# Kernel optimization log

Hardware: AMD Instinct MI355X
Metric: run time of the kernel (lower is better)

The kernel has to match this reference:

```python
import jax, jax.numpy as jnp
import numpy as np

TOP_K = 50  # init default top_k=50
EPS = 1e-12  # torch F.normalize eps


def setup_inputs() -> dict:
    key = jax.random.key(0)
    k1, k2, k3, k4 = jax.random.split(key, 4)
    d = 128
    P = 2048      # number of test patches
    M = 100000    # memory bank size
    return {
        "test_patches": jax.random.normal(k1, (P, d), jnp.float32),
        "memory_nodes": jax.random.normal(k2, (M, d), jnp.float32),
        "W1": jax.random.normal(k3, (d, d // 2), jnp.float32) * 0.05,
        "b1": jnp.zeros((d // 2,), jnp.float32),
        "W2": jax.random.normal(k4, (d // 2, 1), jnp.float32) * 0.05,
        "b2": jnp.zeros((1,), jnp.float32),
    }


def reference(test_patches, memory_nodes, W1, b1, W2, b2):
    P = test_patches.shape[0]
    M = memory_nodes.shape[0]
    K = min(TOP_K, M)

    # --- compute_exact_topk_edges ---
    sim = test_patches @ memory_nodes.T              # [P, M] dense similarity
    _, topk_idx = jax.lax.top_k(sim, K)              # [P, K], sorted descending like torch.topk
    test_idx = jnp.broadcast_to(jnp.arange(P, dtype=topk_idx.dtype)[:, None], (P, K)).reshape(-1)
    edge_index = jnp.stack([topk_idx.reshape(-1), test_idx], axis=0)  # [2, P*K] (memory_idx, test_idx)

    # --- token_evidence_pooling (on test_patches) ---
    logits = jax.nn.relu(test_patches @ W1 + b1) @ W2 + b2  # [P, 1]
    weights = jax.nn.softmax(logits, axis=0)                 # softmax over patches
    g = jnp.sum(test_patches * weights, axis=0, keepdims=True)  # [1, d]
    g = g / jnp.maximum(jnp.linalg.norm(g, axis=-1, keepdims=True), EPS)
    return edge_index, g
```

## Files before the change

### kernel.cpp

```cpp
#include <hip/hip_runtime.h>
#include <math.h>

#define D    128
#define PN   2048
#define MN   100000
#define KK   50
#define NEGF (-3.0e38f)
#define NCB  784
#define NTILE 6272
#define TPW  49
#define CPW  784
#define NRB  16
#define NCP  128
#define SCAP 16
#define PB_CVTB 6272
#define PB_CVTA (PB_CVTB + 128)
#define PB_ALL  (PB_CVTA + 512)

typedef __attribute__((ext_vector_type(8))) short short8;
typedef __attribute__((ext_vector_type(4))) float f32x4;

__device__ __forceinline__ bool pgtf(float va, int ia, float vb, int ib) {
  return (va > vb) || (va == vb && ia < ib);
}

__device__ __forceinline__ unsigned short f2bf(float x) {
  union { float f; unsigned u; } c; c.f = x;
  unsigned r = c.u + 0x7FFFu + ((c.u >> 16) & 1u);
  return (unsigned short)(r >> 16);
}

#define CHAIN_Q(Aj, bj)                                                        \
  do {                                                                         \
    ae = __builtin_fmaf((Aj).x, (bj).x, ae); ao = __builtin_fmaf((Aj).y, (bj).y, ao); \
    ae = __builtin_fmaf((Aj).z, (bj).z, ae); ao = __builtin_fmaf((Aj).w, (bj).w, ao); \
  } while (0)

__global__ __launch_bounds__(256)
void k_prep(const float* __restrict__ X, const float* __restrict__ Bn,
            const float* __restrict__ W1, const float* __restrict__ b1,
            const float* __restrict__ W2, const float* __restrict__ b2,
            short* __restrict__ Ap, short* __restrict__ Bp,
            float* __restrict__ logits) {
  __shared__ float part[4][16];
  const int b   = blockIdx.x;
  const int tid = threadIdx.x;

  if (b < PB_CVTB) {
    int q = b * 256 + tid;
    int cb = q >> 11, t = q & 2047;
    int ct = t >> 8, ks = (t >> 6) & 3, l = t & 63;
    int n  = cb * 128 + ct * 16 + (l & 15);
    int k0 = ks * 32 + (l >> 4) * 8;
    short8 h = {0, 0, 0, 0, 0, 0, 0, 0};
    if (n < MN) {
      const float4* s = (const float4*)(Bn + (size_t)n * D + k0);
      float4 f0 = s[0], f1 = s[1];
      h[0]=(short)f2bf(f0.x); h[1]=(short)f2bf(f0.y); h[2]=(short)f2bf(f0.z); h[3]=(short)f2bf(f0.w);
      h[4]=(short)f2bf(f1.x); h[5]=(short)f2bf(f1.y); h[6]=(short)f2bf(f1.z); h[7]=(short)f2bf(f1.w);
    }
    *(short8*)(Bp + (size_t)q * 8) = h;
  } else if (b < PB_CVTA) {
    int bb = b - PB_CVTB;
    int rb = bb >> 3, rt = bb & 7;
    int ks = tid >> 6, hi = (tid >> 4) & 3, rsel = tid & 15;
    int m  = rb * 128 + rt * 16 + rsel;
    int k0 = ks * 32 + hi * 8;
    const float4* sp = (const float4*)(X + (size_t)m * D + k0);
    float4 f0 = sp[0], f1 = sp[1];
    float ss = f0.x*f0.x + f0.y*f0.y + f0.z*f0.z + f0.w*f0.w
             + f1.x*f1.x + f1.y*f1.y + f1.z*f1.z + f1.w*f1.w;
    ss += __shfl_xor(ss, 16, 64);
    ss += __shfl_xor(ss, 32, 64);
    if ((tid & 63) < 16) part[ks][rsel] = ss;
    __syncthreads();
    float tot = part[0][rsel] + part[1][rsel] + part[2][rsel] + part[3][rsel];
    float rinv = 1.0f / (3.0f * sqrtf(tot));
    short8 h;
    h[0]=(short)f2bf(f0.x*rinv); h[1]=(short)f2bf(f0.y*rinv);
    h[2]=(short)f2bf(f0.z*rinv); h[3]=(short)f2bf(f0.w*rinv);
    h[4]=(short)f2bf(f1.x*rinv); h[5]=(short)f2bf(f1.y*rinv);
    h[6]=(short)f2bf(f1.z*rinv); h[7]=(short)f2bf(f1.w*rinv);
    *(short8*)(Ap + (size_t)(bb * 256 + tid) * 8) = h;
  } else {
    int w = tid >> 6, lane = tid & 63;
    int p = (b - PB_CVTA) * 4 + w;
    const float* xp = X + (size_t)p * D;
    double h = (double)b1[lane];
#pragma unroll 4
    for (int k = 0; k < D; ++k) h += (double)xp[k] * (double)W1[k * 64 + lane];
    float hf = fmaxf((float)h, 0.f);
    double y = (double)hf * (double)W2[lane];
#pragma unroll
    for (int s = 32; s > 0; s >>= 1) y += __shfl_xor(y, s, 64);
    if (lane == 0) logits[p] = (float)(y + (double)b2[0]);
  }
}

__global__ __launch_bounds__(256, 2)
void k_sim(const short* __restrict__ Ap, const short* __restrict__ Bp,
           const float* __restrict__ X, const float* __restrict__ Bn,
           unsigned short* __restrict__ cand2, unsigned char* __restrict__ cnt2,
           float* __restrict__ sco2) {
  __shared__ int lcnt[4][128];

  const int tid  = threadIdx.x;
  const int lane = tid & 63;
  const int wv   = __builtin_amdgcn_readfirstlane(tid >> 6);
  const int xq = blockIdx.x & 7, kq = blockIdx.x >> 3;
  const int w  = xq * 16 + (kq & 15);
  const int g  = kq >> 4;
  const int rb = g * 4 + wv;
  const int row0 = rb * 128;

  lcnt[wv][lane] = 0; lcnt[wv][lane + 64] = 0;
  __syncthreads();

  const int coll = lane & 15;
  const int rql  = (lane >> 4) * 4;

  short8 a[8][4];
  const short8* gA = (const short8*)(Ap + (size_t)rb * 16384);
#pragma unroll
  for (int rt = 0; rt < 8; ++rt)
#pragma unroll
    for (int ks = 0; ks < 4; ++ks)
      a[rt][ks] = gA[(rt * 4 + ks) * 64 + lane];

  const int wbase = w * TPW;
  const f32x4 cinit = {-1.f, -1.f, -1.f, -1.f};

  auto loadB = [&](short8* dst, int s) {
    const short8* gB = (const short8*)Bp + (size_t)(wbase + s) * 256 + lane;
#pragma unroll
    for (int ks = 0; ks < 4; ++ks) dst[ks] = gB[ks * 64];
  };

  auto step = [&](const short8* bf, int s) {
    f32x4 acc[8];
#pragma unroll
    for (int rt = 0; rt < 8; ++rt)
      acc[rt] = __builtin_amdgcn_mfma_f32_16x16x32_bf16(a[rt][0], bf[0], cinit, 0, 0, 0);
#pragma unroll
    for (int ks = 1; ks < 4; ++ks)
#pragma unroll
      for (int rt = 0; rt < 8; ++rt)
        acc[rt] = __builtin_amdgcn_mfma_f32_16x16x32_bf16(a[rt][ks], bf[ks], acc[rt], 0, 0, 0);

    unsigned miss = 0;
#pragma unroll
    for (int rt = 0; rt < 8; ++rt)
#pragma unroll
      for (int rg = 0; rg < 4; ++rg)
        miss |= (__float_as_uint(acc[rt][rg]) >> 31) << (unsigned)(rt * 4 + rg);
    unsigned m0 = ~miss;
    if (m0) {
      int gc = (wbase + s) * 16 + coll;
      unsigned short code = (unsigned short)(s * 16 + coll);
#pragma unroll 1
      while (m0) {
        int b2 = __builtin_ctz(m0); m0 &= m0 - 1;
        int rt = b2 >> 2, rg = b2 & 3;
        if (gc < MN) {
          int row_l = rt * 16 + rql + rg;
          int pos = atomicAdd(&lcnt[wv][row_l], 1);
          if (pos < SCAP) {
            size_t strip = (size_t)(row0 + row_l) * NCP + w;
            cand2[strip * SCAP + pos] = code;
          }
        }
      }
    }
  };

  short8 u[4], v[4];
  loadB(u, 0);
#pragma unroll 1
  for (int s = 0; s < TPW - 1; s += 2) {
    loadB(v, s + 1);
    step(u, s);
    loadB(u, s + 2);
    step(v, s + 1);
  }
  step(u, TPW - 1);

  __syncthreads();

#pragma unroll
  for (int rr = 0; rr < 2; ++rr) {
    int r = rr * 64 + lane;
    int cc = lcnt[wv][r]; if (cc > SCAP) cc = SCAP;
    cnt2[(size_t)(row0 + r) * NCP + w] = (unsigned char)cc;
  }

  const int rrow = tid & 127;
  const int half = tid >> 7;
#pragma unroll 1
  for (int wv2 = 0; wv2 < 4; ++wv2) {
    int cc = lcnt[wv2][rrow]; if (cc > SCAP) cc = SCAP;
    int rowg = (g * 4 + wv2) * 128 + rrow;
    size_t strip = (size_t)rowg * NCP + w;
    const float4* Ar = (const float4*)(X + (size_t)rowg * D);
#pragma unroll 1
    for (int q = half; q < cc; q += 2) {
      int code = cand2[strip * SCAP + q];
      int gcn  = w * CPW + code;
      const float4* Br = (const float4*)(Bn + (size_t)gcn * D);
      float ae = 0.f, ao = 0.f;
#pragma unroll 2
      for (int kb = 0; kb < 8; ++kb) {
        float4 a0 = Ar[kb * 4 + 0], a1 = Ar[kb * 4 + 1],
               a2 = Ar[kb * 4 + 2], a3 = Ar[kb * 4 + 3];
        float4 b0 = Br[kb * 4 + 0], b1 = Br[kb * 4 + 1],
               b2 = Br[kb * 4 + 2], b3 = Br[kb * 4 + 3];
        CHAIN_Q(a0, b0); CHAIN_Q(a1, b1); CHAIN_Q(a2, b2); CHAIN_Q(a3, b3);
      }
      sco2[strip * SCAP + q] = ae + ao;
    }
  }
}

__global__ __launch_bounds__(512)
void k_select(const unsigned short* __restrict__ cand2, const unsigned char* __restrict__ cnt2,
              const float* __restrict__ sco2,
              const float* __restrict__ A,
              const float* __restrict__ logits, float* __restrict__ out) {
  __shared__ int   ixsh[512];
  __shared__ float svsh[512];
  __shared__ int   nsh;
  __shared__ float  wsum2[2048];
  __shared__ double redp[512];
  __shared__ double gpart[128];

  const int tid  = threadIdx.x;
  const int lane = tid & 63;

  if (blockIdx.x == 0) {
    float lv[4];
    float mx = NEGF;
#pragma unroll
    for (int j = 0; j < 4; ++j) { lv[j] = logits[j * 512 + tid]; mx = fmaxf(mx, lv[j]); }
    redp[tid] = (double)mx;
    __syncthreads();
    for (int s = 256; s > 0; s >>= 1) { if (tid < s) redp[tid] = fmax(redp[tid], redp[tid + s]); __syncthreads(); }
    float m = (float)redp[0];
    __syncthreads();
    double ssum = 0.0;
#pragma unroll
    for (int j = 0; j < 4; ++j) {
      float e = expf(lv[j] - m);
      wsum2[j * 512 + tid] = e;
      ssum += (double)e;
    }
    redp[tid] = ssum;
    __syncthreads();
    for (int s = 256; s > 0; s >>= 1) { if (tid < s) redp[tid] += redp[tid + s]; __syncthreads(); }
    double S = redp[0];
    __syncthreads();
    int dim = tid & 127, q = tid >> 7;
    const float* xq = A + (size_t)(q * 512) * D + dim;
    double acc = 0.0;
#pragma unroll 4
    for (int p = 0; p < 512; ++p) acc += (double)wsum2[q * 512 + p] * (double)xq[(size_t)p * D];
    redp[tid] = acc;
    __syncthreads();
    if (tid < 128) {
      double g = (redp[tid] + redp[tid + 128] + redp[tid + 256] + redp[tid + 384]) / S;
      gpart[tid] = g;
      redp[tid] = g * g;
    }
    __syncthreads();
    for (int s = 64; s > 0; s >>= 1) { if (tid < s) redp[tid] += redp[tid + s]; __syncthreads(); }
    if (tid < 128) {
      double nrm = sqrt(redp[0]);
      out[(size_t)2 * PN * KK + tid] = (float)(gpart[tid] / fmax(nrm, 1e-12));
    }
    return;
  }

  const int row = blockIdx.x - 1;

  if (tid < 64) {
    size_t s0 = (size_t)row * NCP + lane;
    size_t s1 = s0 + 64;
    int c0 = cnt2[s0], c1 = cnt2[s1];
    int x = c0 + c1, incl = x;
#pragma unroll
    for (int d2 = 1; d2 < 64; d2 <<= 1) {
      int y = __shfl_up(incl, d2, 64);
      if (lane >= d2) incl += y;
    }
    int off = incl - x;
    int n = __shfl(incl, 63, 64);
    if (n > 512) n = 512;
#pragma unroll 1
    for (int q = 0; q < c0; ++q) {
      int pos = off + q;
      if (pos < 512) {
        ixsh[pos] = lane * CPW + cand2[s0 * SCAP + q];
        svsh[pos] = sco2[s0 * SCAP + q];
      }
    }
#pragma unroll 1
    for (int q = 0; q < c1; ++q) {
      int pos = off + c0 + q;
      if (pos < 512) {
        ixsh[pos] = (lane + 64) * CPW + cand2[s1 * SCAP + q];
        svsh[pos] = sco2[s1 * SCAP + q];
      }
    }
    if (lane == 0) nsh = n;
  }
  __syncthreads();
  const int n = nsh;

  float v; int i;
  if (tid < n) { v = svsh[tid]; i = ixsh[tid]; }
  else         { v = NEGF;      i = 0x40000000 + tid; }

#pragma unroll
  for (int size = 2; size <= 512; size <<= 1) {
#pragma unroll
    for (int stride = size >> 1; stride > 0; stride >>= 1) {
      const bool desc = ((tid & size) == 0);
      if (stride >= 64) {
        __syncthreads();
        svsh[tid] = v; ixsh[tid] = i;
        __syncthreads();
        int p = tid ^ stride;
        float pv = svsh[p]; int pi = ixsh[p];
        bool lower = (tid & stride) == 0;
        bool g = lower ? pgtf(pv, pi, v, i) : pgtf(v, i, pv, pi);
        if (g == desc) { v = pv; i = pi; }
      } else {
        float pv = __shfl_xor(v, stride, 64);
        int   pi = __shfl_xor(i, stride, 64);
        bool lower = (lane & stride) == 0;
        bool g = lower ? pgtf(pv, pi, v, i) : pgtf(v, i, pv, pi);
        if (g == desc) { v = pv; i = pi; }
      }
    }
  }

  if (tid < KK) {
    out[(size_t)row * KK + tid] = (float)i;
    out[(size_t)(PN * KK) + (size_t)row * KK + tid] = (float)row;
  }
}

extern "C" void kernel_launch(void* const* d_in, const int* in_sizes, int n_in,
                              void* d_out, int out_size, void* d_ws, size_t ws_size,
                              hipStream_t stream) {
  const float* X  = (const float*)d_in[0];
  const float* Bn = (const float*)d_in[1];
  const float* W1 = (const float*)d_in[2];
  const float* b1 = (const float*)d_in[3];
  const float* W2 = (const float*)d_in[4];
  const float* b2 = (const float*)d_in[5];
  float* out = (float*)d_out;

  char* p = (char*)d_ws;
  unsigned short* cand2 = (unsigned short*)p; p += (size_t)PN * NCP * SCAP * 2;
  unsigned char*  cnt2  = (unsigned char*)p;  p += (size_t)PN * NCP;
  float* sco2   = (float*)p;                  p += (size_t)PN * NCP * SCAP * 4;
  float* logits = (float*)p;                  p += (size_t)PN * 4;
  short* Ap     = (short*)p;                  p += (size_t)NRB * 2048 * 8 * 2;
  short* Bp     = (short*)p;

  k_prep<<<PB_ALL, 256, 0, stream>>>(X, Bn, W1, b1, W2, b2, Ap, Bp, logits);
  k_sim<<<512, 256, 0, stream>>>(Ap, Bp, X, Bn, cand2, cnt2, sco2);
  k_select<<<PN + 1, 512, 0, stream>>>(cand2, cnt2, sco2, X, logits, out);
}
```

Before: 239.6 us.

## Move exact fp32 rescoring into column-bucketed kernel to reuse memory rows

The fp32 rescoring of bf16 candidates moves out of k_sim. k_sim now appends each candidate's slot index to a per-memory-column list using atomics. A new k_rescore kernel then gives one thread per memory column, which loads that column's row once and dots it against every test patch that picked it. This is meant to cut scattered reloads of memory-bank rows. In exchange it adds a memset, atomics, a large column-list buffer, an extra launch, and a per-column cap of 32 that could drop candidates.

```diff
diff --git a/kernel.cpp b/kernel.cpp
--- a/kernel.cpp
+++ b/kernel.cpp
@@ -7,12 +7,14 @@
 #define KK   50
 #define NEGF (-3.0e38f)
 #define NCB  784
+#define NCOL (NCB * 128)
 #define NTILE 6272
 #define TPW  49
 #define CPW  784
 #define NRB  16
 #define NCP  128
 #define SCAP 16
+#define CCAP 32
 #define PB_CVTB 6272
 #define PB_CVTA (PB_CVTB + 128)
 #define PB_ALL  (PB_CVTA + 512)
@@ -99,9 +101,8 @@
 
 __global__ __launch_bounds__(256, 2)
 void k_sim(const short* __restrict__ Ap, const short* __restrict__ Bp,
-           const float* __restrict__ X, const float* __restrict__ Bn,
            unsigned short* __restrict__ cand2, unsigned char* __restrict__ cnt2,
-           float* __restrict__ sco2) {
+           int* __restrict__ colcnt, unsigned* __restrict__ colList) {
   __shared__ int lcnt[4][128];
 
   const int tid  = threadIdx.x;
@@ -193,30 +194,48 @@
     cnt2[(size_t)(row0 + r) * NCP + w] = (unsigned char)cc;
   }
 
-  const int rrow = tid & 127;
-  const int half = tid >> 7;
-#pragma unroll 1
-  for (int wv2 = 0; wv2 < 4; ++wv2) {
+#pragma unroll 1
+  for (int rr2 = 0; rr2 < 2; ++rr2) {
+    int sr   = rr2 * 256 + tid;
+    int wv2  = sr >> 7, rrow = sr & 127;
     int cc = lcnt[wv2][rrow]; if (cc > SCAP) cc = SCAP;
     int rowg = (g * 4 + wv2) * 128 + rrow;
     size_t strip = (size_t)rowg * NCP + w;
-    const float4* Ar = (const float4*)(X + (size_t)rowg * D);
-#pragma unroll 1
-    for (int q = half; q < cc; q += 2) {
+#pragma unroll 1
+    for (int q = 0; q < cc; ++q) {
       int code = cand2[strip * SCAP + q];
       int gcn  = w * CPW + code;
-      const float4* Br = (const float4*)(Bn + (size_t)gcn * D);
-      float ae = 0.f, ao = 0.f;
+      int pos  = atomicAdd(&colcnt[gcn], 1);
+      if (pos < CCAP) colList[(size_t)gcn * CCAP + pos] = (unsigned)(strip * SCAP + q);
+    }
+  }
+}
+
+__global__ __launch_bounds__(256)
+void k_rescore(const int* __restrict__ colcnt, const unsigned* __restrict__ colList,
+               const float* __restrict__ X, const float* __restrict__ Bn,
+               float* __restrict__ sco2) {
+  const int col = blockIdx.x * 256 + threadIdx.x;
+  if (col >= NCOL) return;
+  int cc = colcnt[col];
+  if (cc <= 0) return;
+  if (cc > CCAP) cc = CCAP;
+  const float4* Br = (const float4*)(Bn + (size_t)col * D);
+#pragma unroll 1
+  for (int q = 0; q < cc; ++q) {
+    unsigned li = colList[(size_t)col * CCAP + q];
+    int row = (int)(li >> 11);
+    const float4* Ar = (const float4*)(X + (size_t)row * D);
+    float ae = 0.f, ao = 0.f;
 #pragma unroll 2
-      for (int kb = 0; kb < 8; ++kb) {
-        float4 a0 = Ar[kb * 4 + 0], a1 = Ar[kb * 4 + 1],
-               a2 = Ar[kb * 4 + 2], a3 = Ar[kb * 4 + 3];
-        float4 b0 = Br[kb * 4 + 0], b1 = Br[kb * 4 + 1],
-               b2 = Br[kb * 4 + 2], b3 = Br[kb * 4 + 3];
-        CHAIN_Q(a0, b0); CHAIN_Q(a1, b1); CHAIN_Q(a2, b2); CHAIN_Q(a3, b3);
-      }
-      sco2[strip * SCAP + q] = ae + ao;
-    }
+    for (int kb = 0; kb < 8; ++kb) {
+      float4 a0 = Ar[kb * 4 + 0], a1 = Ar[kb * 4 + 1],
+             a2 = Ar[kb * 4 + 2], a3 = Ar[kb * 4 + 3];
+      float4 b0 = Br[kb * 4 + 0], b1 = Br[kb * 4 + 1],
+             b2 = Br[kb * 4 + 2], b3 = Br[kb * 4 + 3];
+      CHAIN_Q(a0, b0); CHAIN_Q(a1, b1); CHAIN_Q(a2, b2); CHAIN_Q(a3, b3);
+    }
+    sco2[li] = ae + ao;
   }
 }
 
@@ -362,12 +381,16 @@
   char* p = (char*)d_ws;
   unsigned short* cand2 = (unsigned short*)p; p += (size_t)PN * NCP * SCAP * 2;
   unsigned char*  cnt2  = (unsigned char*)p;  p += (size_t)PN * NCP;
-  float* sco2   = (float*)p;                  p += (size_t)PN * NCP * SCAP * 4;
+  float*    sco2   = (float*)p;               p += (size_t)PN * NCP * SCAP * 4;
+  int*      colcnt = (int*)p;                 p += (size_t)NCOL * 4;
+  unsigned* colList = (unsigned*)p;           p += (size_t)NCOL * CCAP * 4;
   float* logits = (float*)p;                  p += (size_t)PN * 4;
   short* Ap     = (short*)p;                  p += (size_t)NRB * 2048 * 8 * 2;
   short* Bp     = (short*)p;
 
+  hipMemsetAsync(colcnt, 0, (size_t)NCOL * 4, stream);
   k_prep<<<PB_ALL, 256, 0, stream>>>(X, Bn, W1, b1, W2, b2, Ap, Bp, logits);
-  k_sim<<<512, 256, 0, stream>>>(Ap, Bp, X, Bn, cand2, cnt2, sco2);
+  k_sim<<<512, 256, 0, stream>>>(Ap, Bp, cand2, cnt2, colcnt, colList);
+  k_rescore<<<(NCOL + 255) / 256, 256, 0, stream>>>(colcnt, colList, X, Bn, sco2);
   k_select<<<PN + 1, 512, 0, stream>>>(cand2, cnt2, sco2, X, logits, out);
 }
```

Result: slower. 282.9 us (+18.1%).
